# Kernel tuning notes

Hardware: AMD Instinct MI355X
Metric: run time of the kernel (lower is better)

The kernel has to match this reference:

```python
import jax, jax.numpy as jnp
import numpy as np

TEMP = 0.07
LAMBDA_CON = 1.0
LAMBDA_SHELL = 1.0
NEG_INF = -1e30


def setup_inputs() -> dict:
    key = jax.random.key(0)
    k1, k2, k3, k4, k5 = jax.random.split(key, 5)
    B, D = 8192, 1024
    emb = jax.random.normal(k1, (B, D), jnp.float32)
    emb = emb / jnp.linalg.norm(emb, axis=1, keepdims=True)  # encoder outputs are unit-norm
    center = jax.random.normal(k2, (D,), jnp.float32)
    center = center / jnp.linalg.norm(center)  # buffer is F.normalize'd in estimate_epoch_geometry
    labels = jax.random.randint(k3, (B,), 0, 2)  # 0 = machine, 1 = human
    radius_m = jax.random.uniform(k4, (1,), jnp.float32)
    radius_h = radius_m + jax.random.uniform(k5, (1,), jnp.float32)  # radius_h >= radius_m by construction
    return {"embeddings": emb, "center": center, "radius_m": radius_m,
            "radius_h": radius_h, "labels": labels}


def reference(embeddings, center, radius_m, radius_h, labels):
    rm = radius_m[0]
    rh = radius_h[0]
    B = embeddings.shape[0]

    # ---- shell loss ----
    distances = jnp.linalg.norm(embeddings - center[None, :], axis=1)  # [B]
    mmask = labels == 0
    hmask = labels == 1
    nm = jnp.sum(mmask)
    nh = jnp.sum(hmask)
    loss_m = jnp.sum(jnp.where(mmask, jnp.square(jax.nn.relu(distances - rm)), 0.0)) / jnp.maximum(nm, 1)
    loss_h = jnp.sum(jnp.where(hmask, jnp.square(jax.nn.relu(rh - distances)), 0.0)) / jnp.maximum(nh, 1)
    loss_shell = loss_m + loss_h

    # ---- contrastive loss (batched: one BxB sim matrix instead of per-anchor loop) ----
    S = (embeddings @ embeddings.T) / TEMP          # [B, B] pairwise logits
    Sp = (embeddings @ center) / TEMP               # [B]  logits vs prototype
    eye = jnp.eye(B, dtype=bool)
    S_masked = jnp.where(eye, jnp.asarray(NEG_INF, S.dtype), S)
    # denominator per machine anchor i: logsumexp over {other machines, prototype, humans}
    # (labels are only 0/1, so all j != i contribute) plus the prototype logit
    lse = jnp.logaddexp(jax.nn.logsumexp(S_masked, axis=1), Sp)  # [B]
    # positives for machine anchor i: other machines (nm-1) + prototype -> nm positives
    pos_sum = jnp.sum(jnp.where(mmask[None, :] & ~eye, S, 0.0), axis=1) + Sp  # [B]
    anchor_loss = lse - pos_sum / jnp.maximum(nm, 1)
    con_sum = jnp.sum(jnp.where(mmask, anchor_loss, 0.0))
    # prototype as anchor: positives = machines, negatives = humans
    lse_p = jax.nn.logsumexp(Sp)
    proto_loss = lse_p - jnp.sum(jnp.where(mmask, Sp, 0.0)) / jnp.maximum(nm, 1)
    loss_con = (con_sum + proto_loss) / jnp.maximum(nm + 1, 1)
    # original returns 0 when either class is empty
    both = (nm > 0) & (nh > 0)
    loss_con = jnp.where(both, loss_con, 0.0)

    loss = LAMBDA_SHELL * loss_shell + LAMBDA_CON * loss_con
    return (loss, loss_shell, loss_m, loss_h, loss_con, distances)
```

## Files before the change

kernel.cpp:

```cpp
#include <hip/hip_runtime.h>

#define INV_T 14.285714285714286f
#define C1 0.055803571428571425f

typedef float f32x16 __attribute__((ext_vector_type(16)));
typedef float f32x4 __attribute__((ext_vector_type(4)));
typedef int i32x4v __attribute__((ext_vector_type(4)));
typedef int i32x8 __attribute__((ext_vector_type(8)));

__device__ __forceinline__ unsigned char f2e4m3(float f) {
    unsigned char s = (unsigned char)((__float_as_uint(f) >> 24) & 0x80);
    float a = fabsf(f);
    if (a > 448.f) a = 448.f;
    if (a == 0.f) return s;
    int e = (int)((__float_as_uint(a) >> 23) & 0xFF) - 127;
    if (e < -10) return s;
    if (e < -6) e = -6;
    float scale = __int_as_float((unsigned)(130 - e) << 23);
    int mi = (int)rintf(a * scale);
    if (mi >= 16) { mi >>= 1; ++e; }
    if (mi < 8) return s | (unsigned char)mi;
    return s | (unsigned char)(((e + 7) << 3) | (mi - 8));
}

__device__ __forceinline__ void async16(void* l, const void* g) {
    __builtin_amdgcn_global_load_lds(
        (const __attribute__((address_space(1))) unsigned int*)g,
        (__attribute__((address_space(3))) unsigned int*)l, 16, 0, 0);
}

__global__ void __launch_bounds__(256) k_prepcs(const float* __restrict__ emb,
                                                const float* __restrict__ center,
                                                const int* __restrict__ labels,
                                                unsigned char* __restrict__ embQ,
                                                float* __restrict__ out,
                                                float* __restrict__ Sp,
                                                float* __restrict__ s_mp,
                                                float* __restrict__ sumexp,
                                                float* __restrict__ scal,
                                                unsigned* __restrict__ done_ctr,
                                                int D) {
    int t = threadIdx.x;
    int wave = t >> 6, lane = t & 63;
    int nw = blockDim.x >> 6;
    int r0 = blockIdx.x * 8;

    if (t < 8) sumexp[blockIdx.x * 8 + t] = 0.f;
    if (blockIdx.x == 0) {
        if (t < 12) scal[t] = 0.f;
        if (t == 12) *done_ctr = 0u;
    }

    float4 c = ((const float4*)center)[t];

    float4 e[8];
#pragma unroll
    for (int r = 0; r < 8; ++r)
        e[r] = ((const float4*)(emb + (size_t)(r0 + r) * D))[t];
    int lab[8];
#pragma unroll
    for (int r = 0; r < 8; ++r) lab[r] = labels[r0 + r];

    if (embQ) {
#pragma unroll
        for (int r = 0; r < 8; ++r) {
#if __has_builtin(__builtin_amdgcn_cvt_pk_fp8_f32)
            int p = 0;
            p = __builtin_amdgcn_cvt_pk_fp8_f32(e[r].x * 16.f, e[r].y * 16.f, p, false);
            p = __builtin_amdgcn_cvt_pk_fp8_f32(e[r].z * 16.f, e[r].w * 16.f, p, true);
            ((int*)(embQ + (size_t)(r0 + r) * D))[t] = p;
#else
            ((uchar4*)(embQ + (size_t)(r0 + r) * D))[t] =
                make_uchar4(f2e4m3(e[r].x * 16.f), f2e4m3(e[r].y * 16.f),
                            f2e4m3(e[r].z * 16.f), f2e4m3(e[r].w * 16.f));
#endif
        }
    }

    float d2p[8], spp[8];
    float4 colacc = {0.f, 0.f, 0.f, 0.f};
#pragma unroll
    for (int r = 0; r < 8; ++r) {
        float sc = (lab[r] == 0) ? 1.f : 0.f;
        float dx = e[r].x - c.x, dy = e[r].y - c.y,
              dz = e[r].z - c.z, dw = e[r].w - c.w;
        d2p[r] = dx * dx + dy * dy + dz * dz + dw * dw;
        spp[r] = e[r].x * c.x + e[r].y * c.y + e[r].z * c.z + e[r].w * c.w;
        colacc.x += e[r].x * sc; colacc.y += e[r].y * sc;
        colacc.z += e[r].z * sc; colacc.w += e[r].w * sc;
    }

#pragma unroll
    for (int m = 1; m <= 32; m <<= 1)
#pragma unroll
        for (int r = 0; r < 8; ++r) {
            d2p[r] += __shfl_xor(d2p[r], m, 64);
            spp[r] += __shfl_xor(spp[r], m, 64);
        }
    __shared__ float redD[8][4];
    __shared__ float redS[8][4];
    if (lane == 0)
#pragma unroll
        for (int r = 0; r < 8; ++r) { redD[r][wave] = d2p[r]; redS[r][wave] = spp[r]; }

    ((float4*)(s_mp + (size_t)blockIdx.x * D))[t] = colacc;

    __syncthreads();
    if (t < 8) {
        float d2 = 0.f, sp = 0.f;
        for (int w = 0; w < nw; ++w) { d2 += redD[t][w]; sp += redS[t][w]; }
        out[5 + r0 + t] = sqrtf(d2);
        Sp[r0 + t] = sp * INV_T;
    }
}

#define MXMFMA(a, b, c) __builtin_amdgcn_mfma_scale_f32_32x32x64_f8f6f4( \
    (a), (b), (c), 0, 0, 0, 0x7F7F7F7F, 0, 0x7F7F7F7F)

__global__ void __launch_bounds__(256, 2)
k_sumexp_mx(const unsigned char* __restrict__ embQ, float* __restrict__ sumexp,
            int D, int nT) {
    const int n = nT;
    int nwg = n * (n + 1) / 2;
    int bid = blockIdx.x;
    if ((nwg & 7) == 0) {
        int cpx = nwg >> 3;
        bid = (bid & 7) * cpx + (bid >> 3);
    }
    float nf = (float)n + 0.5f;
    int rb = (int)(nf - sqrtf(fmaxf(nf * nf - 2.0f * (float)bid, 0.f)));
    if (rb < 0) rb = 0;
    if (rb > n - 1) rb = n - 1;
#define TRI_OFF(r) ((r) * n - ((r) * ((r)-1)) / 2)
    while (rb + 1 <= n - 1 && TRI_OFF(rb + 1) <= bid) ++rb;
    while (rb > 0 && TRI_OFF(rb) > bid) --rb;
    int cb = rb + (bid - TRI_OFF(rb));
#undef TRI_OFF
    int rowbase = rb * 128, colbase = cb * 128;

    int tid = threadIdx.x;
    int wave = tid >> 6, lane = tid & 63;
    int wr = wave >> 1, wc = wave & 1;
    int l31 = lane & 31, kk = lane >> 5;

    __shared__ unsigned char sA[2][16384];
    __shared__ unsigned char sB[2][16384];
    __shared__ float rred[2][128];
    __shared__ float cred[2][128];

    f32x16 acc[2][2];
#pragma unroll
    for (int fr = 0; fr < 2; ++fr)
#pragma unroll
        for (int fc = 0; fc < 2; ++fc)
#pragma unroll
            for (int v = 0; v < 16; ++v) acc[fr][fc][v] = 0.f;

    const int kG = D >> 7;

    const unsigned char* gSA[4];
    const unsigned char* gSB[4];
    unsigned int dstOff[4];
#pragma unroll
    for (int q = 0; q < 4; ++q) {
        int ch = q * 256 + tid;
        int row = ch >> 3, lc = ch & 7;
        int gc = lc ^ (row & 7);
        gSA[q] = embQ + (size_t)(rowbase + row) * D + gc * 16;
        gSB[q] = embQ + (size_t)(colbase + row) * D + gc * 16;
        dstOff[q] = (unsigned)ch << 4;
    }

    auto stage = [&](int buf, int kt) {
        int ko = kt << 7;
#pragma unroll
        for (int q = 0; q < 4; ++q) {
            async16(&sA[buf][dstOff[q]], gSA[q] + ko);
            async16(&sB[buf][dstOff[q]], gSB[q] + ko);
        }
    };

    int e7 = (l31 & 7) << 4;
    int offs[2][2];
#pragma unroll
    for (int h = 0; h < 2; ++h)
#pragma unroll
        for (int j = 0; j < 2; ++j)
            offs[h][j] = (((h * 4 + kk * 2 + j) << 4) ^ e7);
    int aBase0 = (wr * 64 + l31) << 7;
    int aBase1 = aBase0 + (32 << 7);
    int bBase0 = (wc * 64 + l31) << 7;
    int bBase1 = bBase0 + (32 << 7);

    stage(0, 0);
    for (int kt = 0; kt < kG; ++kt) {
        int cur = kt & 1;
        __syncthreads();
        if (kt + 1 < kG) stage(cur ^ 1, kt + 1);
        const unsigned char* A = sA[cur];
        const unsigned char* Bp = sB[cur];
#pragma unroll
        for (int h = 0; h < 2; ++h) {
            i32x8 av[2], bv[2];
            {
                i32x4v lo = *(const i32x4v*)&A[aBase0 + offs[h][0]];
                i32x4v hi = *(const i32x4v*)&A[aBase0 + offs[h][1]];
                av[0] = __builtin_shufflevector(lo, hi, 0, 1, 2, 3, 4, 5, 6, 7);
            }
            {
                i32x4v lo = *(const i32x4v*)&A[aBase1 + offs[h][0]];
                i32x4v hi = *(const i32x4v*)&A[aBase1 + offs[h][1]];
                av[1] = __builtin_shufflevector(lo, hi, 0, 1, 2, 3, 4, 5, 6, 7);
            }
            {
                i32x4v lo = *(const i32x4v*)&Bp[bBase0 + offs[h][0]];
                i32x4v hi = *(const i32x4v*)&Bp[bBase0 + offs[h][1]];
                bv[0] = __builtin_shufflevector(lo, hi, 0, 1, 2, 3, 4, 5, 6, 7);
            }
            {
                i32x4v lo = *(const i32x4v*)&Bp[bBase1 + offs[h][0]];
                i32x4v hi = *(const i32x4v*)&Bp[bBase1 + offs[h][1]];
                bv[1] = __builtin_shufflevector(lo, hi, 0, 1, 2, 3, 4, 5, 6, 7);
            }
#pragma unroll
            for (int fr = 0; fr < 2; ++fr)
#pragma unroll
                for (int fc = 0; fc < 2; ++fc)
                    acc[fr][fc] = MXMFMA(av[fr], bv[fc], acc[fr][fc]);
        }
    }

    float rs[2][16];
    float cs[2] = {0.f, 0.f};
#pragma unroll
    for (int fr = 0; fr < 2; ++fr)
#pragma unroll
        for (int v = 0; v < 16; ++v) rs[fr][v] = 0.f;

#pragma unroll
    for (int fr = 0; fr < 2; ++fr)
#pragma unroll
        for (int fc = 0; fc < 2; ++fc) {
            int gcol = colbase + wc * 64 + fc * 32 + l31;
#pragma unroll
            for (int v = 0; v < 16; ++v) {
                int grow = rowbase + wr * 64 + fr * 32 + (v & 3) + 8 * (v >> 2) + 4 * kk;
                float e = (grow < gcol) ? __expf(acc[fr][fc][v] * C1 - INV_T) : 0.f;
                rs[fr][v] += e;
                cs[fc] += e;
            }
        }

#pragma unroll
    for (int m = 1; m <= 16; m <<= 1)
#pragma unroll
        for (int fr = 0; fr < 2; ++fr)
#pragma unroll
            for (int v = 0; v < 16; ++v) rs[fr][v] += __shfl_xor(rs[fr][v], m, 64);
    if (l31 == 0)
#pragma unroll
        for (int fr = 0; fr < 2; ++fr)
#pragma unroll
            for (int v = 0; v < 16; ++v)
                rred[wc][wr * 64 + fr * 32 + (v & 3) + 8 * (v >> 2) + 4 * kk] = rs[fr][v];

#pragma unroll
    for (int fc = 0; fc < 2; ++fc) cs[fc] += __shfl_xor(cs[fc], 32, 64);
    if (kk == 0)
#pragma unroll
        for (int fc = 0; fc < 2; ++fc) cred[wr][wc * 64 + fc * 32 + l31] = cs[fc];

    __syncthreads();
    if (tid < 128) {
        atomicAdd(&sumexp[rowbase + tid], rred[0][tid] + rred[1][tid]);
    } else {
        int u = tid - 128;
        atomicAdd(&sumexp[colbase + u], cred[0][u] + cred[1][u]);
    }
}

typedef __bf16 bf16x8 __attribute__((ext_vector_type(8)));
typedef unsigned short u16x8 __attribute__((ext_vector_type(8)));
__device__ __forceinline__ unsigned short f2bf(float f) {
    unsigned int x = __float_as_uint(f);
    x += 0x7fffu + ((x >> 16) & 1u);
    return (unsigned short)(x >> 16);
}
__global__ void __launch_bounds__(256) k_sumexp_fb(const float* __restrict__ embF,
                                                   float* __restrict__ sumexp, int D, int nTiles) {
    int bid = blockIdx.x;
    const int n = nTiles;
    float nf = (float)n + 0.5f;
    int rb = (int)(nf - sqrtf(fmaxf(nf * nf - 2.0f * (float)bid, 0.f)));
    if (rb < 0) rb = 0;
    if (rb > n - 1) rb = n - 1;
#define TRI_OFF(r) ((r) * n - ((r) * ((r)-1)) / 2)
    while (rb + 1 <= n - 1 && TRI_OFF(rb + 1) <= bid) ++rb;
    while (rb > 0 && TRI_OFF(rb) > bid) --rb;
    int cb = rb + (bid - TRI_OFF(rb));
#undef TRI_OFF
    int tid = threadIdx.x;
    int wave = tid >> 6, lane = tid & 63;
    int wr = wave >> 1, wc = wave & 1;
    int quad = lane >> 4, l15 = lane & 15;
    int rowbase = rb * 128, colbase = cb * 128;
    __shared__ unsigned short lA[128 * 64];
    __shared__ unsigned short lB[128 * 64];
    __shared__ float rred[2][128];
    __shared__ float cred[2][128];
    f32x4 zero = {0.f, 0.f, 0.f, 0.f};
    f32x4 acc[4][4];
#pragma unroll
    for (int r = 0; r < 4; ++r)
#pragma unroll
        for (int c = 0; c < 4; ++c) acc[r][c] = zero;
    const int kIters = D >> 6;
    for (int kt = 0; kt < kIters; ++kt) {
        int k0 = kt << 6;
#pragma unroll
        for (int q = 0; q < 4; ++q) {
            int ch = q * 256 + tid;
            int row = ch >> 3, lc = ch & 7;
            int pc = lc ^ (row & 7);
            const float4* sa = (const float4*)(embF + (size_t)(rowbase + row) * D + k0 + lc * 8);
            const float4* sb = (const float4*)(embF + (size_t)(colbase + row) * D + k0 + lc * 8);
            float4 a0 = sa[0], a1 = sa[1];
            float4 b0 = sb[0], b1 = sb[1];
            u16x8 va = {f2bf(a0.x), f2bf(a0.y), f2bf(a0.z), f2bf(a0.w),
                        f2bf(a1.x), f2bf(a1.y), f2bf(a1.z), f2bf(a1.w)};
            u16x8 vb = {f2bf(b0.x), f2bf(b0.y), f2bf(b0.z), f2bf(b0.w),
                        f2bf(b1.x), f2bf(b1.y), f2bf(b1.z), f2bf(b1.w)};
            *(u16x8*)&lA[(row << 6) + (pc << 3)] = va;
            *(u16x8*)&lB[(row << 6) + (pc << 3)] = vb;
        }
        __syncthreads();
#pragma unroll
        for (int h = 0; h < 2; ++h) {
            bf16x8 af[4], bfr[4];
#pragma unroll
            for (int r = 0; r < 4; ++r) {
                int row = wr * 64 + r * 16 + l15;
                int pc = (h * 4 + quad) ^ (l15 & 7);
                af[r] = *(const bf16x8*)&lA[(row << 6) + (pc << 3)];
            }
#pragma unroll
            for (int c = 0; c < 4; ++c) {
                int row = wc * 64 + c * 16 + l15;
                int pc = (h * 4 + quad) ^ (l15 & 7);
                bfr[c] = *(const bf16x8*)&lB[(row << 6) + (pc << 3)];
            }
#pragma unroll
            for (int r = 0; r < 4; ++r)
#pragma unroll
                for (int c = 0; c < 4; ++c)
                    acc[r][c] = __builtin_amdgcn_mfma_f32_16x16x32_bf16(af[r], bfr[c], acc[r][c], 0, 0, 0);
        }
        __syncthreads();
    }
    float rs[4][4], cs[4];
#pragma unroll
    for (int r = 0; r < 4; ++r)
#pragma unroll
        for (int v = 0; v < 4; ++v) rs[r][v] = 0.f;
#pragma unroll
    for (int c = 0; c < 4; ++c) cs[c] = 0.f;
#pragma unroll
    for (int r = 0; r < 4; ++r)
#pragma unroll
        for (int c = 0; c < 4; ++c) {
            f32x4 a = acc[r][c];
            int gcol = colbase + wc * 64 + c * 16 + l15;
#pragma unroll
            for (int v = 0; v < 4; ++v) {
                int grow = rowbase + wr * 64 + r * 16 + quad * 4 + v;
                float e = (grow < gcol) ? __expf((a[v] - 1.0f) * INV_T) : 0.f;
                rs[r][v] += e;
                cs[c] += e;
            }
        }
#pragma unroll
    for (int m = 1; m <= 8; m <<= 1)
#pragma unroll
        for (int r = 0; r < 4; ++r)
#pragma unroll
            for (int v = 0; v < 4; ++v) rs[r][v] += __shfl_xor(rs[r][v], m, 64);
    if (l15 == 0)
#pragma unroll
        for (int r = 0; r < 4; ++r)
#pragma unroll
            for (int v = 0; v < 4; ++v)
                rred[wc][wr * 64 + r * 16 + quad * 4 + v] = rs[r][v];
#pragma unroll
    for (int m = 16; m <= 32; m <<= 1)
#pragma unroll
        for (int c = 0; c < 4; ++c) cs[c] += __shfl_xor(cs[c], m, 64);
    if (quad == 0)
#pragma unroll
        for (int c = 0; c < 4; ++c) cred[wr][wc * 64 + c * 16 + l15] = cs[c];
    __syncthreads();
    if (tid < 128) {
        atomicAdd(&sumexp[rowbase + tid], rred[0][tid] + rred[1][tid]);
    } else {
        int u = tid & 127;
        atomicAdd(&sumexp[colbase + u], cred[0][u] + cred[1][u]);
    }
}

__global__ void __launch_bounds__(256) k_fin(const float* __restrict__ Sp,
                                             const float* __restrict__ sumexp,
                                             const int* __restrict__ labels,
                                             const float* __restrict__ outv,
                                             const float* __restrict__ s_mp,
                                             const float* __restrict__ center,
                                             const float* __restrict__ rmp,
                                             const float* __restrict__ rhp,
                                             float* __restrict__ scal,
                                             unsigned* __restrict__ done_ctr,
                                             float* __restrict__ out,
                                             int D, int B, int nPart) {
    int t = threadIdx.x, lane = t & 63, wave = t >> 6;
    int i = blockIdx.x * blockDim.x + t;
    float rm = rmp[0], rh = rhp[0];
    float a[9];
#pragma unroll
    for (int k = 0; k < 9; ++k) a[k] = 0.f;
    if (i < B) {
        float LP = Sp[i];
        float eS = __expf(LP - INV_T);
        float lse = INV_T + __logf(sumexp[i] + eS);
        float d = outv[5 + i];
        bool mach = (labels[i] == 0);
        a[2] = eS;
        if (mach) {
            a[4] = lse; a[3] = LP; a[5] = d * d; a[8] = 1.f;
            float x = d - rm; a[0] = (x > 0.f) ? x * x : 0.f;
        } else {
            float x = rh - d; a[1] = (x > 0.f) ? x * x : 0.f;
        }
    }
    if (blockIdx.x == 0)
        for (int j = t; j < D; j += blockDim.x) { float cv = center[j]; a[7] += cv * cv; }
    __shared__ float sacc[8][33];
    int pg = t >> 5, dl = t & 31;
    for (int dbase = blockIdx.x * 32; dbase < D; dbase += gridDim.x * 32) {
        int d = dbase + dl;
        float accp = 0.f;
        if (d < D)
            for (int p = pg; p < nPart; p += 8) accp += s_mp[(size_t)p * D + d];
        sacc[pg][dl] = accp;
        __syncthreads();
        if (t < 32 && dbase + t < D) {
            float s = sacc[0][t] + sacc[1][t] + sacc[2][t] + sacc[3][t] +
                      sacc[4][t] + sacc[5][t] + sacc[6][t] + sacc[7][t];
            a[6] += s * s;
        }
        __syncthreads();
    }
#pragma unroll
    for (int m = 1; m <= 32; m <<= 1)
#pragma unroll
        for (int k = 0; k < 9; ++k) a[k] += __shfl_xor(a[k], m, 64);
    __shared__ float red[4][9];
    if (lane == 0)
#pragma unroll
        for (int k = 0; k < 9; ++k) red[wave][k] = a[k];
    __syncthreads();
    if (t < 9) {
        float v = red[0][t] + red[1][t] + red[2][t] + red[3][t];
        atomicAdd(&scal[t], v);
    }
    __syncthreads();
    if (t == 0) {
        __threadfence();
        unsigned done = atomicAdd(done_ctr, 1u);
        if (done == (unsigned)gridDim.x - 1) {
            __threadfence();
            float s[9];
#pragma unroll
            for (int k = 0; k < 9; ++k) s[k] = atomicAdd(&scal[k], 0.f);
            int nm = (int)(s[8] + 0.5f);
            int nh = B - nm;
            float nmf = (float)(nm > 1 ? nm : 1);
            float nhf = (float)(nh > 1 ? nh : 1);
            float loss_m = s[0] / nmf;
            float loss_h = s[1] / nhf;
            float loss_shell = loss_m + loss_h;
            float lse_p = INV_T + __logf(s[2]);
            float proto = lse_p - s[3] / nmf;
            float sum_sd = s[5] + 2.f * s[3] / INV_T - (float)nm * s[7];
            float pos_m = INV_T * (s[6] - sum_sd) + s[3];
            float con = s[4] - pos_m / nmf;
            int denom = (nm + 1 > 1) ? nm + 1 : 1;
            float lc = (con + proto) / (float)denom;
            if (!(nm > 0 && nh > 0)) lc = 0.f;
            out[0] = loss_shell + lc;
            out[1] = loss_shell;
            out[2] = loss_m;
            out[3] = loss_h;
            out[4] = lc;
        }
    }
}

extern "C" void kernel_launch(void* const* d_in, const int* in_sizes, int n_in,
                              void* d_out, int out_size, void* d_ws, size_t ws_size,
                              hipStream_t stream) {
    const float* emb = (const float*)d_in[0];
    const float* center = (const float*)d_in[1];
    const float* rmp = (const float*)d_in[2];
    const float* rhp = (const float*)d_in[3];
    const int* labels = (const int*)d_in[4];
    float* out = (float*)d_out;
    const int B = in_sizes[4];
    const int D = in_sizes[1];

    const int nPart = B / 8;
    size_t qBytes = (size_t)B * D;
    size_t partBytes = (size_t)nPart * D * 4;
    size_t auxBytes = (size_t)B * 4 + (size_t)B * 4 + 64 + partBytes;
    bool pre = (ws_size >= qBytes + auxBytes) && (B % 128 == 0) &&
               (D % 128 == 0) && (D <= 1024);
    size_t Z0 = pre ? qBytes : 0;

    char* ws = (char*)d_ws;
    unsigned char* embQ = (unsigned char*)ws;
    float* sumexp = (float*)(ws + Z0);
    float* Sp = (float*)(ws + Z0 + (size_t)B * 4);
    float* scal = (float*)(ws + Z0 + (size_t)B * 8);
    unsigned* done_ctr = (unsigned*)(scal + 12);
    float* s_mp = (float*)(ws + Z0 + (size_t)B * 8 + 64);

    k_prepcs<<<B / 8, D / 4, 0, stream>>>(emb, center, labels,
                                          pre ? embQ : nullptr, out, Sp, s_mp,
                                          sumexp, scal, done_ctr, D);

    int nT = B / 128;
    int nBlocks = nT * (nT + 1) / 2;
    if (pre) k_sumexp_mx<<<nBlocks, 256, 0, stream>>>(embQ, sumexp, D, nT);
    else     k_sumexp_fb<<<nBlocks, 256, 0, stream>>>(emb, sumexp, D, nT);

    k_fin<<<(B + 255) / 256, 256, 0, stream>>>(Sp, sumexp, labels, out, s_mp,
                                               center, rmp, rhp, scal,
                                               done_ctr, out, D, B, nPart);
}
```

Before: 196.0 us.

## Split prep kernel into quantize and geometry kernels, halve partial column sums

```diff
diff --git a/kernel.cpp b/kernel.cpp
--- a/kernel.cpp
+++ b/kernel.cpp
@@ -29,84 +29,91 @@
         (__attribute__((address_space(3))) unsigned int*)l, 16, 0, 0);
 }
 
-__global__ void __launch_bounds__(256) k_prepcs(const float* __restrict__ emb,
-                                                const float* __restrict__ center,
-                                                const int* __restrict__ labels,
-                                                unsigned char* __restrict__ embQ,
-                                                float* __restrict__ out,
-                                                float* __restrict__ Sp,
-                                                float* __restrict__ s_mp,
-                                                float* __restrict__ sumexp,
-                                                float* __restrict__ scal,
-                                                unsigned* __restrict__ done_ctr,
-                                                int D) {
+
+__global__ void __launch_bounds__(256) k_quant(const float* __restrict__ emb,
+                                               unsigned char* __restrict__ embQ,
+                                               float* __restrict__ sumexp,
+                                               float* __restrict__ scal,
+                                               unsigned* __restrict__ done_ctr,
+                                               int D) {
     int t = threadIdx.x;
-    int wave = t >> 6, lane = t & 63;
-    int nw = blockDim.x >> 6;
     int r0 = blockIdx.x * 8;
-
     if (t < 8) sumexp[blockIdx.x * 8 + t] = 0.f;
     if (blockIdx.x == 0) {
         if (t < 12) scal[t] = 0.f;
         if (t == 12) *done_ctr = 0u;
     }
-
-    float4 c = ((const float4*)center)[t];
-
     float4 e[8];
 #pragma unroll
     for (int r = 0; r < 8; ++r)
         e[r] = ((const float4*)(emb + (size_t)(r0 + r) * D))[t];
-    int lab[8];
-#pragma unroll
-    for (int r = 0; r < 8; ++r) lab[r] = labels[r0 + r];
-
-    if (embQ) {
+#pragma unroll
+    for (int r = 0; r < 8; ++r) {
+#if __has_builtin(__builtin_amdgcn_cvt_pk_fp8_f32)
+        int p = 0;
+        p = __builtin_amdgcn_cvt_pk_fp8_f32(e[r].x * 16.f, e[r].y * 16.f, p, false);
+        p = __builtin_amdgcn_cvt_pk_fp8_f32(e[r].z * 16.f, e[r].w * 16.f, p, true);
+        ((int*)(embQ + (size_t)(r0 + r) * D))[t] = p;
+#else
+        ((uchar4*)(embQ + (size_t)(r0 + r) * D))[t] =
+            make_uchar4(f2e4m3(e[r].x * 16.f), f2e4m3(e[r].y * 16.f),
+                        f2e4m3(e[r].z * 16.f), f2e4m3(e[r].w * 16.f));
+#endif
+    }
+}
+
+__global__ void __launch_bounds__(256) k_geom(const float* __restrict__ emb,
+                                              const float* __restrict__ center,
+                                              const int* __restrict__ labels,
+                                              float* __restrict__ out,
+                                              float* __restrict__ Sp,
+                                              float* __restrict__ s_mp,
+                                              int D) {
+    int t = threadIdx.x;
+    int wave = t >> 6, lane = t & 63;
+    int nw = blockDim.x >> 6;
+    int r0 = blockIdx.x * 16;
+    float4 c = ((const float4*)center)[t];
+    float d2p[16], spp[16];
+    float4 colacc = {0.f, 0.f, 0.f, 0.f};
+#pragma unroll
+    for (int g = 0; g < 2; ++g) {
+        int rbase = r0 + g * 8;
+        float4 e[8];
+#pragma unroll
+        for (int r = 0; r < 8; ++r)
+            e[r] = ((const float4*)(emb + (size_t)(rbase + r) * D))[t];
+        int lab[8];
+#pragma unroll
+        for (int r = 0; r < 8; ++r) lab[r] = labels[rbase + r];
 #pragma unroll
         for (int r = 0; r < 8; ++r) {
-#if __has_builtin(__builtin_amdgcn_cvt_pk_fp8_f32)
-            int p = 0;
-            p = __builtin_amdgcn_cvt_pk_fp8_f32(e[r].x * 16.f, e[r].y * 16.f, p, false);
-            p = __builtin_amdgcn_cvt_pk_fp8_f32(e[r].z * 16.f, e[r].w * 16.f, p, true);
-            ((int*)(embQ + (size_t)(r0 + r) * D))[t] = p;
-#else
-            ((uchar4*)(embQ + (size_t)(r0 + r) * D))[t] =
-                make_uchar4(f2e4m3(e[r].x * 16.f), f2e4m3(e[r].y * 16.f),
-                            f2e4m3(e[r].z * 16.f), f2e4m3(e[r].w * 16.f));
-#endif
-        }
-    }
-
-    float d2p[8], spp[8];
-    float4 colacc = {0.f, 0.f, 0.f, 0.f};
-#pragma unroll
-    for (int r = 0; r < 8; ++r) {
-        float sc = (lab[r] == 0) ? 1.f : 0.f;
-        float dx = e[r].x - c.x, dy = e[r].y - c.y,
-              dz = e[r].z - c.z, dw = e[r].w - c.w;
-        d2p[r] = dx * dx + dy * dy + dz * dz + dw * dw;
-        spp[r] = e[r].x * c.x + e[r].y * c.y + e[r].z * c.z + e[r].w * c.w;
-        colacc.x += e[r].x * sc; colacc.y += e[r].y * sc;
-        colacc.z += e[r].z * sc; colacc.w += e[r].w * sc;
-    }
-
+            float sc = (lab[r] == 0) ? 1.f : 0.f;
+            float dx = e[r].x - c.x, dy = e[r].y - c.y,
+                  dz = e[r].z - c.z, dw = e[r].w - c.w;
+            d2p[g * 8 + r] = dx * dx + dy * dy + dz * dz + dw * dw;
+            spp[g * 8 + r] = e[r].x * c.x + e[r].y * c.y + e[r].z * c.z + e[r].w * c.w;
+            colacc.x += e[r].x * sc; colacc.y += e[r].y * sc;
+            colacc.z += e[r].z * sc; colacc.w += e[r].w * sc;
+        }
+    }
 #pragma unroll
     for (int m = 1; m <= 32; m <<= 1)
 #pragma unroll
-        for (int r = 0; r < 8; ++r) {
+        for (int r = 0; r < 16; ++r) {
             d2p[r] += __shfl_xor(d2p[r], m, 64);
             spp[r] += __shfl_xor(spp[r], m, 64);
         }
-    __shared__ float redD[8][4];
-    __shared__ float redS[8][4];
+    __shared__ float redD[16][4];
+    __shared__ float redS[16][4];
     if (lane == 0)
 #pragma unroll
-        for (int r = 0; r < 8; ++r) { redD[r][wave] = d2p[r]; redS[r][wave] = spp[r]; }
+        for (int r = 0; r < 16; ++r) { redD[r][wave] = d2p[r]; redS[r][wave] = spp[r]; }
 
     ((float4*)(s_mp + (size_t)blockIdx.x * D))[t] = colacc;
 
     __syncthreads();
-    if (t < 8) {
+    if (t < 16) {
         float d2 = 0.f, sp = 0.f;
         for (int w = 0; w < nw; ++w) { d2 += redD[t][w]; sp += redS[t][w]; }
         out[5 + r0 + t] = sqrtf(d2);
@@ -444,10 +451,16 @@
     int pg = t >> 5, dl = t & 31;
     for (int dbase = blockIdx.x * 32; dbase < D; dbase += gridDim.x * 32) {
         int d = dbase + dl;
-        float accp = 0.f;
-        if (d < D)
-            for (int p = pg; p < nPart; p += 8) accp += s_mp[(size_t)p * D + d];
-        sacc[pg][dl] = accp;
+        float a0 = 0.f, a1 = 0.f, a2 = 0.f, a3 = 0.f;
+        if (d < D) {
+            for (int p = pg; p < nPart; p += 32) {
+                a0 += s_mp[(size_t)p * D + d];
+                a1 += s_mp[(size_t)(p + 8) * D + d];
+                a2 += s_mp[(size_t)(p + 16) * D + d];
+                a3 += s_mp[(size_t)(p + 24) * D + d];
+            }
+        }
+        sacc[pg][dl] = (a0 + a1) + (a2 + a3);
         __syncthreads();
         if (t < 32 && dbase + t < D) {
             float s = sacc[0][t] + sacc[1][t] + sacc[2][t] + sacc[3][t] +
@@ -514,25 +527,29 @@
     const int B = in_sizes[4];
     const int D = in_sizes[1];
 
-    const int nPart = B / 8;
+    const int nPart = B / 16;
     size_t qBytes = (size_t)B * D;
     size_t partBytes = (size_t)nPart * D * 4;
-    size_t auxBytes = (size_t)B * 4 + (size_t)B * 4 + 64 + partBytes;
-    bool pre = (ws_size >= qBytes + auxBytes) && (B % 128 == 0) &&
-               (D % 128 == 0) && (D <= 1024);
+    size_t auxBytes = (size_t)B * 4 + 64 + (size_t)B * 4 + partBytes;
+    bool pre = (ws_size >= qBytes + auxBytes) && (B % 256 == 0) &&
+               (D % 256 == 0) && (D <= 1024);
     size_t Z0 = pre ? qBytes : 0;
 
     char* ws = (char*)d_ws;
     unsigned char* embQ = (unsigned char*)ws;
     float* sumexp = (float*)(ws + Z0);
-    float* Sp = (float*)(ws + Z0 + (size_t)B * 4);
-    float* scal = (float*)(ws + Z0 + (size_t)B * 8);
+    float* scal = (float*)(ws + Z0 + (size_t)B * 4);
     unsigned* done_ctr = (unsigned*)(scal + 12);
-    float* s_mp = (float*)(ws + Z0 + (size_t)B * 8 + 64);
-
-    k_prepcs<<<B / 8, D / 4, 0, stream>>>(emb, center, labels,
-                                          pre ? embQ : nullptr, out, Sp, s_mp,
-                                          sumexp, scal, done_ctr, D);
+    float* Sp = (float*)(ws + Z0 + (size_t)B * 4 + 64);
+    float* s_mp = (float*)(ws + Z0 + (size_t)B * 4 + 64 + (size_t)B * 4);
+
+    if (pre) {
+        k_quant<<<B / 8, D / 4, 0, stream>>>(emb, embQ, sumexp, scal, done_ctr, D);
+    } else {
+        hipMemsetAsync(ws + Z0, 0, (size_t)B * 4 + 64, stream);
+    }
+
+    k_geom<<<B / 16, D / 4, 0, stream>>>(emb, center, labels, out, Sp, s_mp, D);
 
     int nT = B / 128;
     int nBlocks = nT * (nT + 1) / 2;
```

Result: faster. 172.6 us (-11.9%).
